# Kernel optimization log

Hardware: AMD Instinct MI355X
Metric: run time of the kernel (lower is better)

The kernel has to match this reference:

```python
import jax, jax.numpy as jnp
import numpy as np

BETA = 0.001  # commitment loss weight from __init__ default


def setup_inputs() -> dict:
    key = jax.random.key(0)
    k1, k2 = jax.random.split(key)
    N, INPUT_DIM = 8192, 1024
    S, K, D = 32, 1024, 32  # nsplits, num_embeddings, embedding_dim
    z = jax.random.normal(k1, (N, INPUT_DIM), dtype=jnp.float32)
    # Stacked codebook weights: one [K, D] embedding table per split.
    W = jax.random.normal(k2, (S, K, D), dtype=jnp.float32)
    return {"z": z, "W": W}


def reference(z, W):
    N, INPUT_DIM = z.shape
    S, K, D = W.shape
    zc = z.reshape(N, S, D)  # per-split chunks, matches torch.chunk(z, S, -1)
    # Squared euclidean distances ||z||^2 + ||w||^2 - 2 z.w  -> [N, S, K]
    d2 = (
        jnp.sum(zc * zc, axis=-1, keepdims=True)
        + jnp.sum(W * W, axis=-1)[None, :, :]
        - 2.0 * jnp.einsum("nsd,skd->nsk", zc, W)
    )
    idx = jnp.argmin(d2, axis=-1)  # [N, S]
    # Gather nearest codes: W[s, idx[n, s]] -> [N, S, D]
    zq = W[jnp.arange(S)[None, :], idx]
    # Sum over splits of per-split mse means; equal split sizes so this is
    # S * mean over the whole tensor.
    sg = jax.lax.stop_gradient
    loss = S * (
        jnp.mean((sg(zq) - zc) ** 2) + BETA * jnp.mean((zq - sg(zc)) ** 2)
    )
    # Straight-through estimator
    zq_st = zc + sg(zq - zc)
    return zq_st.reshape(N, INPUT_DIM), loss
```

## Files before the change

kernel.cpp:

```cpp
#include <hip/hip_runtime.h>
#include <math.h>

#define NN 8192
#define SS 32
#define DD 32
#define KK 1024
#define OUT_ELEMS ((size_t)NN * SS * DD)

#define LOSS_SCALE (32.0f * 1.001f / 8388608.0f)

typedef _Float16 half8 __attribute__((ext_vector_type(8)));
typedef float   floatx4 __attribute__((ext_vector_type(4)));

#define NTILES 64
#define RG 2
#define WAVES 16
#define BLK_ROWS (WAVES * RG * 16)
#define NBLOCKS ((NN / BLK_ROWS) * SS)


#define W2P_OFF  4096
#define WHP_OFF  (W2P_OFF + SS * KK * 4)
#define WLP_OFF  (WHP_OFF + SS * KK * DD * 2)

typedef const __attribute__((address_space(1))) void* gas_p;
typedef __attribute__((address_space(3))) void* las_p;

__device__ __forceinline__ void gll16(const void* g, void* l) {
    __builtin_amdgcn_global_load_lds((gas_p)g, (las_p)l, 16, 0, 0);
}
__device__ __forceinline__ void gll4(const void* g, void* l) {
    __builtin_amdgcn_global_load_lds((gas_p)g, (las_p)l, 4, 0, 0);
}

__global__ __launch_bounds__(256) void w_pre(const float* __restrict__ W,
                                             _Float16* __restrict__ WhP,
                                             _Float16* __restrict__ WlP,
                                             float* __restrict__ w2P) {
    const int u    = blockIdx.x * 256 + threadIdx.x;
    const int s    = u >> 12;
    const int g    = (u >> 6) & 63;
    const int l    = u & 63;
    const int col  = l & 15;
    const int quad = l >> 4;
    const int k    = g * 16 + col;
    const float* src = W + ((size_t)s * KK + k) * DD + quad * 8;
    const float4 va = ((const float4*)src)[0];
    const float4 vb = ((const float4*)src)[1];
    const float v[8] = {va.x, va.y, va.z, va.w, vb.x, vb.y, vb.z, vb.w};
    half8 h8, l8; float ps = 0.0f;
    #pragma unroll
    for (int j = 0; j < 8; ++j) {
        const float x = v[j];
        ps = fmaf(x, x, ps);
        const _Float16 h = (_Float16)x;
        h8[j] = h;
        l8[j] = (_Float16)(x - (float)h);
    }
    ps += __shfl_xor(ps, 16, 64);
    ps += __shfl_xor(ps, 32, 64);
    *(half8*)(WhP + (size_t)u * 8) = h8;
    *(half8*)(WlP + (size_t)u * 8) = l8;
    if (quad == 0) w2P[s * KK + k] = ps;
}

__global__ __launch_bounds__(1024, 4) void vq_fused(const float* __restrict__ z,
                                                    const float* __restrict__ W,
                                                    const _Float16* __restrict__ WhP,
                                                    const _Float16* __restrict__ WlP,
                                                    const float* __restrict__ w2P,
                                                    float* __restrict__ out,
                                                    float* __restrict__ part) {
    __shared__ _Float16 bufH[NTILES][64][8];
    __shared__ _Float16 bufL[NTILES][64][8];
    __shared__ float    w2b[KK];
    __shared__ int      lds_idx[WAVES][32];
    __shared__ float    lds_part[WAVES];

    const int s    = blockIdx.x & (SS - 1);
    const int n0b  = (blockIdx.x >> 5) * BLK_ROWS;
    const int tid  = threadIdx.x;
    const int wv   = tid >> 6;
    const int lane = tid & 63;
    const int col  = lane & 15;
    const int quad = lane >> 4;

    const float* __restrict__ Ws = W + (size_t)s * KK * DD;
    const int n0w = n0b + wv * (RG * 16);

    {
        const char* gH = (const char*)(WhP + (size_t)s * (NTILES * 512));
        const char* gL = (const char*)(WlP + (size_t)s * (NTILES * 512));
        char* lH = (char*)&bufH[0][0][0];
        char* lL = (char*)&bufL[0][0][0];
        const int wvB = wv * 1024;
        #pragma unroll
        for (int i = 0; i < 4; ++i) {
            const int off = i * 16384 + wvB;
            gll16(gH + off + lane * 16, lH + off);
            gll16(gL + off + lane * 16, lL + off);
        }
        const float* g2 = w2P + (size_t)s * KK + wv * 64;
        gll4(g2 + lane, (char*)w2b + wv * 256);
    }

    half8 zh[RG], zl[RG];
    #pragma unroll
    for (int rg = 0; rg < RG; ++rg) {
        const float* zp = z + (size_t)(n0w + rg * 16 + col) * (SS * DD) + s * DD + quad * 8;
        const float4 va = ((const float4*)zp)[0];
        const float4 vb = ((const float4*)zp)[1];
        const float src[8] = {va.x, va.y, va.z, va.w, vb.x, vb.y, vb.z, vb.w};
        #pragma unroll
        for (int j = 0; j < 8; ++j) {
            const float v = -2.0f * src[j];
            const _Float16 h = (_Float16)v;
            zh[rg][j] = h;
            zl[rg][j] = (_Float16)(v - (float)h);
        }
    }

    floatx4 best[RG];
    int bi[RG][4];
    #pragma unroll
    for (int rg = 0; rg < RG; ++rg) {
        best[rg] = (floatx4){INFINITY, INFINITY, INFINITY, INFINITY};
        bi[rg][0] = bi[rg][1] = bi[rg][2] = bi[rg][3] = 0;
    }

    __syncthreads();

    #pragma unroll 8
    for (int tt = 0; tt < NTILES; ++tt) {
        const half8 bh = *(const half8*)&bufH[tt][lane][0];
        const half8 bl = *(const half8*)&bufL[tt][lane][0];
        const float w2v = w2b[tt * 16 + col];
        const floatx4 c0 = {w2v, w2v, w2v, w2v};
        __builtin_amdgcn_s_setprio(1);
        floatx4 a0 = __builtin_amdgcn_mfma_f32_16x16x32_f16(zh[0], bh, c0, 0, 0, 0);
        floatx4 a1 = __builtin_amdgcn_mfma_f32_16x16x32_f16(zh[1], bh, c0, 0, 0, 0);
        a0 = __builtin_amdgcn_mfma_f32_16x16x32_f16(zl[0], bh, a0, 0, 0, 0);
        a1 = __builtin_amdgcn_mfma_f32_16x16x32_f16(zl[1], bh, a1, 0, 0, 0);
        a0 = __builtin_amdgcn_mfma_f32_16x16x32_f16(zh[0], bl, a0, 0, 0, 0);
        a1 = __builtin_amdgcn_mfma_f32_16x16x32_f16(zh[1], bl, a1, 0, 0, 0);
        __builtin_amdgcn_s_setprio(0);
        #pragma unroll
        for (int i = 0; i < 4; ++i) {
            if (a0[i] < best[0][i]) { best[0][i] = a0[i]; bi[0][i] = tt; }
            if (a1[i] < best[1][i]) { best[1][i] = a1[i]; bi[1][i] = tt; }
        }
    }

    #pragma unroll
    for (int rg = 0; rg < RG; ++rg) {
        #pragma unroll
        for (int i = 0; i < 4; ++i) {
            float v = best[rg][i];
            int   k = bi[rg][i] * 16 + col;
            #pragma unroll
            for (int m = 1; m < 16; m <<= 1) {
                const float vo = __shfl_xor(v, m, 64);
                const int   ko = __shfl_xor(k, m, 64);
                if (vo < v || (vo == v && ko < k)) { v = vo; k = ko; }
            }
            if (col == 0) lds_idx[wv][rg * 16 + quad * 4 + i] = k;
        }
    }
    __syncthreads();

    const int r  = lane & 31;
    const int dh = (lane >> 5) * 16;
    const int krow = lds_idx[wv][r];
    const float* wsrc = Ws + (size_t)krow * DD + dh;
    const size_t zoff = (size_t)(n0w + r) * (SS * DD) + s * DD + dh;
    const float* zsrc = z + zoff;
    float* od = out + zoff;
    float sq = 0.0f;
    #pragma unroll
    for (int cc = 0; cc < 4; ++cc) {
        const float4 wq = ((const float4*)wsrc)[cc];
        const float4 zv = ((const float4*)zsrc)[cc];
        const float d0 = wq.x - zv.x, d1 = wq.y - zv.y;
        const float d2 = wq.z - zv.z, d3 = wq.w - zv.w;
        sq = fmaf(d0, d0, sq); sq = fmaf(d1, d1, sq);
        sq = fmaf(d2, d2, sq); sq = fmaf(d3, d3, sq);
        ((float4*)od)[cc] = wq;
    }
    #pragma unroll
    for (int off = 32; off > 0; off >>= 1) sq += __shfl_down(sq, off, 64);

    if (lane == 0) lds_part[wv] = sq;
    __syncthreads();
    if (tid == 0) {
        float t = 0.0f;
        #pragma unroll
        for (int w = 0; w < WAVES; ++w) t += lds_part[w];
        part[blockIdx.x] = t;
    }
}

__global__ __launch_bounds__(256) void vq_loss(const float* __restrict__ part,
                                               float* __restrict__ out) {
    __shared__ float l[4];
    const int tid = threadIdx.x;
    float sum = 0.0f;
    #pragma unroll
    for (int i = 0; i < NBLOCKS / 256; ++i) sum += part[tid + i * 256];
    #pragma unroll
    for (int off = 32; off > 0; off >>= 1) sum += __shfl_down(sum, off, 64);
    if ((tid & 63) == 0) l[tid >> 6] = sum;
    __syncthreads();
    if (tid == 0) out[OUT_ELEMS] = (l[0] + l[1] + l[2] + l[3]) * LOSS_SCALE;
}

extern "C" void kernel_launch(void* const* d_in, const int* in_sizes, int n_in,
                              void* d_out, int out_size, void* d_ws, size_t ws_size,
                              hipStream_t stream) {
    const float* z = (const float*)d_in[0];
    const float* W = (const float*)d_in[1];
    float* out  = (float*)d_out;

    char* ws = (char*)d_ws;
    float*    part = (float*)ws;
    float*    w2P  = (float*)(ws + W2P_OFF);
    _Float16* WhP  = (_Float16*)(ws + WHP_OFF);
    _Float16* WlP  = (_Float16*)(ws + WLP_OFF);

    w_pre<<<dim3(512), dim3(256), 0, stream>>>(W, WhP, WlP, w2P);
    vq_fused<<<dim3(NBLOCKS), dim3(1024), 0, stream>>>(z, W, WhP, WlP, w2P, out, part);
    vq_loss<<<dim3(1), dim3(256), 0, stream>>>(part, out);
}
```

Baseline: 157.3 us.

## Switch distance MFMA from 16x16x32 to 32x32x16 tiles per wave

Replaces the pair of 16x16x32 f16 MFMA row groups with a single 32x32x16 MFMA tile per wave. Each wave covers 32 rows by 32 codes per step over 32 code groups, and the W half/low-part packing is rearranged to the matching layout. The per-tile loop overhead, LDS reads and argmin compare count per code are meant to drop, and the larger MFMA shape may have better throughput. In exchange the 16-element accumulator and the 32-lane cross-lane argmin reduction use more registers and shuffles. The w2 norm is now computed from a separate full-row read in the prep kernel instead of a shuffle reduction.

```diff
diff --git a/kernel.cpp b/kernel.cpp
--- a/kernel.cpp
+++ b/kernel.cpp
@@ -9,13 +9,13 @@
 
 #define LOSS_SCALE (32.0f * 1.001f / 8388608.0f)
 
-typedef _Float16 half8 __attribute__((ext_vector_type(8)));
-typedef float   floatx4 __attribute__((ext_vector_type(4)));
-
-#define NTILES 64
-#define RG 2
+typedef _Float16 half8  __attribute__((ext_vector_type(8)));
+typedef float   floatx4  __attribute__((ext_vector_type(4)));
+typedef float   floatx16 __attribute__((ext_vector_type(16)));
+
+#define NTILES 32
 #define WAVES 16
-#define BLK_ROWS (WAVES * RG * 16)
+#define BLK_ROWS (WAVES * 32)
 #define NBLOCKS ((NN / BLK_ROWS) * SS)
 
 
@@ -32,36 +32,47 @@
 __device__ __forceinline__ void gll4(const void* g, void* l) {
     __builtin_amdgcn_global_load_lds((gas_p)g, (las_p)l, 4, 0, 0);
 }
+
+#define MFMA32(a, b, c) __builtin_amdgcn_mfma_f32_32x32x16_f16((a), (b), (c), 0, 0, 0)
 
 __global__ __launch_bounds__(256) void w_pre(const float* __restrict__ W,
                                              _Float16* __restrict__ WhP,
                                              _Float16* __restrict__ WlP,
                                              float* __restrict__ w2P) {
-    const int u    = blockIdx.x * 256 + threadIdx.x;
-    const int s    = u >> 12;
-    const int g    = (u >> 6) & 63;
-    const int l    = u & 63;
-    const int col  = l & 15;
-    const int quad = l >> 4;
-    const int k    = g * 16 + col;
-    const float* src = W + ((size_t)s * KK + k) * DD + quad * 8;
+    const int u  = blockIdx.x * 256 + threadIdx.x;
+    const int s  = u >> 12;
+    const int r  = u & 4095;
+    const int g  = r >> 7;
+    const int q  = (r >> 6) & 1;
+    const int l  = u & 63;
+    const int k  = g * 32 + (l & 31);
+    const int db = q * 16 + (l >> 5) * 8;
+    const float* src = W + ((size_t)s * KK + k) * DD + db;
     const float4 va = ((const float4*)src)[0];
     const float4 vb = ((const float4*)src)[1];
     const float v[8] = {va.x, va.y, va.z, va.w, vb.x, vb.y, vb.z, vb.w};
-    half8 h8, l8; float ps = 0.0f;
+    half8 h8, l8;
     #pragma unroll
     for (int j = 0; j < 8; ++j) {
         const float x = v[j];
-        ps = fmaf(x, x, ps);
         const _Float16 h = (_Float16)x;
         h8[j] = h;
         l8[j] = (_Float16)(x - (float)h);
     }
-    ps += __shfl_xor(ps, 16, 64);
-    ps += __shfl_xor(ps, 32, 64);
     *(half8*)(WhP + (size_t)u * 8) = h8;
     *(half8*)(WlP + (size_t)u * 8) = l8;
-    if (quad == 0) w2P[s * KK + k] = ps;
+
+    if (u < SS * KK) {
+        const float* row = W + (size_t)u * DD;
+        float ps = 0.0f;
+        #pragma unroll
+        for (int c = 0; c < 8; ++c) {
+            const float4 w4 = ((const float4*)row)[c];
+            ps = fmaf(w4.x, w4.x, ps); ps = fmaf(w4.y, w4.y, ps);
+            ps = fmaf(w4.z, w4.z, ps); ps = fmaf(w4.w, w4.w, ps);
+        }
+        w2P[u] = ps;
+    }
 }
 
 __global__ __launch_bounds__(1024, 4) void vq_fused(const float* __restrict__ z,
@@ -71,8 +82,8 @@
                                                     const float* __restrict__ w2P,
                                                     float* __restrict__ out,
                                                     float* __restrict__ part) {
-    __shared__ _Float16 bufH[NTILES][64][8];
-    __shared__ _Float16 bufL[NTILES][64][8];
+    __shared__ _Float16 bufH[NTILES][2][64][8];
+    __shared__ _Float16 bufL[NTILES][2][64][8];
     __shared__ float    w2b[KK];
     __shared__ int      lds_idx[WAVES][32];
     __shared__ float    lds_part[WAVES];
@@ -82,17 +93,17 @@
     const int tid  = threadIdx.x;
     const int wv   = tid >> 6;
     const int lane = tid & 63;
-    const int col  = lane & 15;
-    const int quad = lane >> 4;
+    const int rowa = lane & 31;
+    const int q5   = lane >> 5;
 
     const float* __restrict__ Ws = W + (size_t)s * KK * DD;
-    const int n0w = n0b + wv * (RG * 16);
+    const int n0w = n0b + wv * 32;
 
     {
-        const char* gH = (const char*)(WhP + (size_t)s * (NTILES * 512));
-        const char* gL = (const char*)(WlP + (size_t)s * (NTILES * 512));
-        char* lH = (char*)&bufH[0][0][0];
-        char* lL = (char*)&bufL[0][0][0];
+        const char* gH = (const char*)(WhP + (size_t)s * (NTILES * 2 * 512));
+        const char* gL = (const char*)(WlP + (size_t)s * (NTILES * 2 * 512));
+        char* lH = (char*)&bufH[0][0][0][0];
+        char* lL = (char*)&bufL[0][0][0][0];
         const int wvB = wv * 1024;
         #pragma unroll
         for (int i = 0; i < 4; ++i) {
@@ -104,72 +115,72 @@
         gll4(g2 + lane, (char*)w2b + wv * 256);
     }
 
-    half8 zh[RG], zl[RG];
-    #pragma unroll
-    for (int rg = 0; rg < RG; ++rg) {
-        const float* zp = z + (size_t)(n0w + rg * 16 + col) * (SS * DD) + s * DD + quad * 8;
+    half8 zh0, zl0, zh1, zl1;
+    {
+        const float* zp = z + (size_t)(n0w + rowa) * (SS * DD) + s * DD + q5 * 8;
         const float4 va = ((const float4*)zp)[0];
         const float4 vb = ((const float4*)zp)[1];
-        const float src[8] = {va.x, va.y, va.z, va.w, vb.x, vb.y, vb.z, vb.w};
+        const float4 vc = ((const float4*)(zp + 16))[0];
+        const float4 vd = ((const float4*)(zp + 16))[1];
+        const float s0[8] = {va.x, va.y, va.z, va.w, vb.x, vb.y, vb.z, vb.w};
+        const float s1[8] = {vc.x, vc.y, vc.z, vc.w, vd.x, vd.y, vd.z, vd.w};
         #pragma unroll
         for (int j = 0; j < 8; ++j) {
-            const float v = -2.0f * src[j];
-            const _Float16 h = (_Float16)v;
-            zh[rg][j] = h;
-            zl[rg][j] = (_Float16)(v - (float)h);
-        }
-    }
-
-    floatx4 best[RG];
-    int bi[RG][4];
-    #pragma unroll
-    for (int rg = 0; rg < RG; ++rg) {
-        best[rg] = (floatx4){INFINITY, INFINITY, INFINITY, INFINITY};
-        bi[rg][0] = bi[rg][1] = bi[rg][2] = bi[rg][3] = 0;
-    }
-
-    __syncthreads();
-
-    #pragma unroll 8
-    for (int tt = 0; tt < NTILES; ++tt) {
-        const half8 bh = *(const half8*)&bufH[tt][lane][0];
-        const half8 bl = *(const half8*)&bufL[tt][lane][0];
-        const float w2v = w2b[tt * 16 + col];
-        const floatx4 c0 = {w2v, w2v, w2v, w2v};
-        __builtin_amdgcn_s_setprio(1);
-        floatx4 a0 = __builtin_amdgcn_mfma_f32_16x16x32_f16(zh[0], bh, c0, 0, 0, 0);
-        floatx4 a1 = __builtin_amdgcn_mfma_f32_16x16x32_f16(zh[1], bh, c0, 0, 0, 0);
-        a0 = __builtin_amdgcn_mfma_f32_16x16x32_f16(zl[0], bh, a0, 0, 0, 0);
-        a1 = __builtin_amdgcn_mfma_f32_16x16x32_f16(zl[1], bh, a1, 0, 0, 0);
-        a0 = __builtin_amdgcn_mfma_f32_16x16x32_f16(zh[0], bl, a0, 0, 0, 0);
-        a1 = __builtin_amdgcn_mfma_f32_16x16x32_f16(zh[1], bl, a1, 0, 0, 0);
-        __builtin_amdgcn_s_setprio(0);
-        #pragma unroll
-        for (int i = 0; i < 4; ++i) {
-            if (a0[i] < best[0][i]) { best[0][i] = a0[i]; bi[0][i] = tt; }
-            if (a1[i] < best[1][i]) { best[1][i] = a1[i]; bi[1][i] = tt; }
-        }
-    }
-
-    #pragma unroll
-    for (int rg = 0; rg < RG; ++rg) {
-        #pragma unroll
-        for (int i = 0; i < 4; ++i) {
-            float v = best[rg][i];
-            int   k = bi[rg][i] * 16 + col;
-            #pragma unroll
-            for (int m = 1; m < 16; m <<= 1) {
-                const float vo = __shfl_xor(v, m, 64);
-                const int   ko = __shfl_xor(k, m, 64);
-                if (vo < v || (vo == v && ko < k)) { v = vo; k = ko; }
-            }
-            if (col == 0) lds_idx[wv][rg * 16 + quad * 4 + i] = k;
-        }
-    }
-    __syncthreads();
-
-    const int r  = lane & 31;
-    const int dh = (lane >> 5) * 16;
+            const float v0 = -2.0f * s0[j];
+            const _Float16 h0 = (_Float16)v0;
+            zh0[j] = h0; zl0[j] = (_Float16)(v0 - (float)h0);
+            const float v1 = -2.0f * s1[j];
+            const _Float16 h1 = (_Float16)v1;
+            zh1[j] = h1; zl1[j] = (_Float16)(v1 - (float)h1);
+        }
+    }
+
+    floatx16 best;
+    int bi[16];
+    #pragma unroll
+    for (int i = 0; i < 16; ++i) { best[i] = INFINITY; bi[i] = 0; }
+
+    __syncthreads();
+
+    #pragma unroll 2
+    for (int g = 0; g < NTILES; ++g) {
+        const half8 bh0 = *(const half8*)&bufH[g][0][lane][0];
+        const half8 bh1 = *(const half8*)&bufH[g][1][lane][0];
+        const half8 bl0 = *(const half8*)&bufL[g][0][lane][0];
+        const half8 bl1 = *(const half8*)&bufL[g][1][lane][0];
+        const float w2v = w2b[g * 32 + rowa];
+        floatx16 c0;
+        #pragma unroll
+        for (int i = 0; i < 16; ++i) c0[i] = w2v;
+        floatx16 acc;
+        acc = MFMA32(zh0, bh0, c0);
+        acc = MFMA32(zh1, bh1, acc);
+        acc = MFMA32(zl0, bh0, acc);
+        acc = MFMA32(zl1, bh1, acc);
+        acc = MFMA32(zh0, bl0, acc);
+        acc = MFMA32(zh1, bl1, acc);
+        #pragma unroll
+        for (int i = 0; i < 16; ++i) {
+            if (acc[i] < best[i]) { best[i] = acc[i]; bi[i] = g; }
+        }
+    }
+
+    #pragma unroll
+    for (int i = 0; i < 16; ++i) {
+        float v = best[i];
+        int   k = bi[i] * 32 + rowa;
+        #pragma unroll
+        for (int m = 1; m < 32; m <<= 1) {
+            const float vo = __shfl_xor(v, m, 64);
+            const int   ko = __shfl_xor(k, m, 64);
+            if (vo < v || (vo == v && ko < k)) { v = vo; k = ko; }
+        }
+        if (rowa == 0) lds_idx[wv][(i & 3) + 8 * (i >> 2) + 4 * q5] = k;
+    }
+    __syncthreads();
+
+    const int r  = rowa;
+    const int dh = q5 * 16;
     const int krow = lds_idx[wv][r];
     const float* wsrc = Ws + (size_t)krow * DD + dh;
     const size_t zoff = (size_t)(n0w + r) * (SS * DD) + s * DD + dh;
```

Measured after the change: 168.9 us. +7.4%, slower.

## Interleave hi/lo codebook tiles and software-pipeline LDS reads with inline asm

Applied to the files above, without the earlier changes.

Codebook hi and lo fp16 halves are now interleaved per tile in one workspace buffer and one LDS array, so a single base address and immediate offsets cover both. The distance loop is hand-pipelined: ds_read_b128/ds_read_b32 are issued via inline asm four tiles ahead with explicit lgkmcnt waits. Each tile's argmin compare is deferred by one tile so it overlaps the next tile's MFMAs. The aim is to hide LDS latency and compare work behind MFMA issue. The cost is fragile inline asm and manual scheduling that may fight the compiler.

```diff
diff --git a/kernel.cpp b/kernel.cpp
--- a/kernel.cpp
+++ b/kernel.cpp
@@ -9,19 +9,17 @@
 
 #define LOSS_SCALE (32.0f * 1.001f / 8388608.0f)
 
-typedef _Float16 half8 __attribute__((ext_vector_type(8)));
+typedef _Float16 half8  __attribute__((ext_vector_type(8)));
 typedef float   floatx4 __attribute__((ext_vector_type(4)));
 
 #define NTILES 64
-#define RG 2
 #define WAVES 16
-#define BLK_ROWS (WAVES * RG * 16)
+#define BLK_ROWS (WAVES * 32)
 #define NBLOCKS ((NN / BLK_ROWS) * SS)
 
 
 #define W2P_OFF  4096
-#define WHP_OFF  (W2P_OFF + SS * KK * 4)
-#define WLP_OFF  (WHP_OFF + SS * KK * DD * 2)
+#define WP_OFF   (W2P_OFF + SS * KK * 4)
 
 typedef const __attribute__((address_space(1))) void* gas_p;
 typedef __attribute__((address_space(3))) void* las_p;
@@ -33,9 +31,10 @@
     __builtin_amdgcn_global_load_lds((gas_p)g, (las_p)l, 4, 0, 0);
 }
 
+#define MFMA16(a, b, c) __builtin_amdgcn_mfma_f32_16x16x32_f16((a), (b), (c), 0, 0, 0)
+
 __global__ __launch_bounds__(256) void w_pre(const float* __restrict__ W,
-                                             _Float16* __restrict__ WhP,
-                                             _Float16* __restrict__ WlP,
+                                             _Float16* __restrict__ WP,
                                              float* __restrict__ w2P) {
     const int u    = blockIdx.x * 256 + threadIdx.x;
     const int s    = u >> 12;
@@ -59,20 +58,19 @@
     }
     ps += __shfl_xor(ps, 16, 64);
     ps += __shfl_xor(ps, 32, 64);
-    *(half8*)(WhP + (size_t)u * 8) = h8;
-    *(half8*)(WlP + (size_t)u * 8) = l8;
+    _Float16* base = WP + ((size_t)(s * 64 + g) * 2) * 512;
+    *(half8*)(base + l * 8) = h8;
+    *(half8*)(base + 512 + l * 8) = l8;
     if (quad == 0) w2P[s * KK + k] = ps;
 }
 
 __global__ __launch_bounds__(1024, 4) void vq_fused(const float* __restrict__ z,
                                                     const float* __restrict__ W,
-                                                    const _Float16* __restrict__ WhP,
-                                                    const _Float16* __restrict__ WlP,
+                                                    const _Float16* __restrict__ WP,
                                                     const float* __restrict__ w2P,
                                                     float* __restrict__ out,
                                                     float* __restrict__ part) {
-    __shared__ _Float16 bufH[NTILES][64][8];
-    __shared__ _Float16 bufL[NTILES][64][8];
+    __shared__ _Float16 bufHL[NTILES][2][64][8];
     __shared__ float    w2b[KK];
     __shared__ int      lds_idx[WAVES][32];
     __shared__ float    lds_part[WAVES];
@@ -86,86 +84,134 @@
     const int quad = lane >> 4;
 
     const float* __restrict__ Ws = W + (size_t)s * KK * DD;
-    const int n0w = n0b + wv * (RG * 16);
+    const int n0w = n0b + wv * 32;
 
     {
-        const char* gH = (const char*)(WhP + (size_t)s * (NTILES * 512));
-        const char* gL = (const char*)(WlP + (size_t)s * (NTILES * 512));
-        char* lH = (char*)&bufH[0][0][0];
-        char* lL = (char*)&bufL[0][0][0];
+        const char* gW = (const char*)(WP + (size_t)s * (NTILES * 2 * 512));
+        char* lW = (char*)&bufHL[0][0][0][0];
         const int wvB = wv * 1024;
         #pragma unroll
-        for (int i = 0; i < 4; ++i) {
+        for (int i = 0; i < 8; ++i) {
             const int off = i * 16384 + wvB;
-            gll16(gH + off + lane * 16, lH + off);
-            gll16(gL + off + lane * 16, lL + off);
+            gll16(gW + off + lane * 16, lW + off);
         }
         const float* g2 = w2P + (size_t)s * KK + wv * 64;
         gll4(g2 + lane, (char*)w2b + wv * 256);
     }
 
-    half8 zh[RG], zl[RG];
-    #pragma unroll
-    for (int rg = 0; rg < RG; ++rg) {
-        const float* zp = z + (size_t)(n0w + rg * 16 + col) * (SS * DD) + s * DD + quad * 8;
-        const float4 va = ((const float4*)zp)[0];
-        const float4 vb = ((const float4*)zp)[1];
-        const float src[8] = {va.x, va.y, va.z, va.w, vb.x, vb.y, vb.z, vb.w};
+    half8 zh0, zl0, zh1, zl1;
+    {
+        const float* zp0 = z + (size_t)(n0w + col) * (SS * DD) + s * DD + quad * 8;
+        const float* zp1 = zp0 + 16 * (SS * DD);
+        const float4 va = ((const float4*)zp0)[0];
+        const float4 vb = ((const float4*)zp0)[1];
+        const float4 vc = ((const float4*)zp1)[0];
+        const float4 vd = ((const float4*)zp1)[1];
+        const float s0[8] = {va.x, va.y, va.z, va.w, vb.x, vb.y, vb.z, vb.w};
+        const float s1[8] = {vc.x, vc.y, vc.z, vc.w, vd.x, vd.y, vd.z, vd.w};
         #pragma unroll
         for (int j = 0; j < 8; ++j) {
-            const float v = -2.0f * src[j];
-            const _Float16 h = (_Float16)v;
-            zh[rg][j] = h;
-            zl[rg][j] = (_Float16)(v - (float)h);
+            const float v0 = -2.0f * s0[j];
+            const _Float16 h0 = (_Float16)v0;
+            zh0[j] = h0; zl0[j] = (_Float16)(v0 - (float)h0);
+            const float v1 = -2.0f * s1[j];
+            const _Float16 h1 = (_Float16)v1;
+            zh1[j] = h1; zl1[j] = (_Float16)(v1 - (float)h1);
         }
     }
 
-    floatx4 best[RG];
-    int bi[RG][4];
-    #pragma unroll
-    for (int rg = 0; rg < RG; ++rg) {
-        best[rg] = (floatx4){INFINITY, INFINITY, INFINITY, INFINITY};
-        bi[rg][0] = bi[rg][1] = bi[rg][2] = bi[rg][3] = 0;
-    }
-
-    __syncthreads();
-
-    #pragma unroll 8
-    for (int tt = 0; tt < NTILES; ++tt) {
-        const half8 bh = *(const half8*)&bufH[tt][lane][0];
-        const half8 bl = *(const half8*)&bufL[tt][lane][0];
-        const float w2v = w2b[tt * 16 + col];
-        const floatx4 c0 = {w2v, w2v, w2v, w2v};
-        __builtin_amdgcn_s_setprio(1);
-        floatx4 a0 = __builtin_amdgcn_mfma_f32_16x16x32_f16(zh[0], bh, c0, 0, 0, 0);
-        floatx4 a1 = __builtin_amdgcn_mfma_f32_16x16x32_f16(zh[1], bh, c0, 0, 0, 0);
-        a0 = __builtin_amdgcn_mfma_f32_16x16x32_f16(zl[0], bh, a0, 0, 0, 0);
-        a1 = __builtin_amdgcn_mfma_f32_16x16x32_f16(zl[1], bh, a1, 0, 0, 0);
-        a0 = __builtin_amdgcn_mfma_f32_16x16x32_f16(zh[0], bl, a0, 0, 0, 0);
-        a1 = __builtin_amdgcn_mfma_f32_16x16x32_f16(zh[1], bl, a1, 0, 0, 0);
-        __builtin_amdgcn_s_setprio(0);
-        #pragma unroll
-        for (int i = 0; i < 4; ++i) {
-            if (a0[i] < best[0][i]) { best[0][i] = a0[i]; bi[0][i] = tt; }
-            if (a1[i] < best[1][i]) { best[1][i] = a1[i]; bi[1][i] = tt; }
-        }
-    }
-
-    #pragma unroll
-    for (int rg = 0; rg < RG; ++rg) {
-        #pragma unroll
-        for (int i = 0; i < 4; ++i) {
-            float v = best[rg][i];
-            int   k = bi[rg][i] * 16 + col;
-            #pragma unroll
-            for (int m = 1; m < 16; m <<= 1) {
-                const float vo = __shfl_xor(v, m, 64);
-                const int   ko = __shfl_xor(k, m, 64);
-                if (vo < v || (vo == v && ko < k)) { v = vo; k = ko; }
-            }
-            if (col == 0) lds_idx[wv][rg * 16 + quad * 4 + i] = k;
-        }
-    }
+    floatx4 best0, best1;
+    int bi0[4], bi1[4];
+    best0 = best1 = (floatx4){INFINITY, INFINITY, INFINITY, INFINITY};
+    bi0[0] = bi0[1] = bi0[2] = bi0[3] = 0;
+    bi1[0] = bi1[1] = bi1[2] = bi1[3] = 0;
+
+    __syncthreads();
+
+    unsigned hladdr = (unsigned)(unsigned long long)(las_p)&bufHL[0][0][0][0]
+                      + (unsigned)(lane * 16);
+    unsigned w2addr = (unsigned)(unsigned long long)(las_p)&w2b[0]
+                      + (unsigned)(col * 4);
+
+#define ISSUE(FH, FL, FW, HO, LO, WO)                                       \
+    asm volatile("ds_read_b128 %0, %3 offset:%c5\n\t"                       \
+                 "ds_read_b128 %1, %3 offset:%c6\n\t"                       \
+                 "ds_read_b32  %2, %4 offset:%c7"                           \
+                 : "=&v"(FH), "=&v"(FL), "=&v"(FW)                          \
+                 : "v"(hladdr), "v"(w2addr), "i"(HO), "i"(LO), "i"(WO))
+
+#define WAITL(N) do {                                                       \
+    asm volatile("s_waitcnt lgkmcnt(%c0)" :: "i"(N) : "memory");            \
+    __builtin_amdgcn_sched_barrier(0);                                      \
+} while (0)
+
+#define MTILE(FH, FL, FW, A0, A1) do {                                      \
+    const floatx4 c0_ = {FW, FW, FW, FW};                                   \
+    A0 = MFMA16(zh0, FH, c0_);                                              \
+    A1 = MFMA16(zh1, FH, c0_);                                              \
+    A0 = MFMA16(zl0, FH, A0);                                               \
+    A1 = MFMA16(zl1, FH, A1);                                               \
+    A0 = MFMA16(zh0, FL, A0);                                               \
+    A1 = MFMA16(zh1, FL, A1);                                               \
+} while (0)
+
+#define CTILE(P0, P1, TK) do {                                              \
+    const int tk_ = (TK);                                                   \
+    _Pragma("unroll")                                                       \
+    for (int i_ = 0; i_ < 4; ++i_) {   \
+        if (P0[i_] < best0[i_]) { best0[i_] = P0[i_]; bi0[i_] = tk_; }      \
+        if (P1[i_] < best1[i_]) { best1[i_] = P1[i_]; bi1[i_] = tk_; }      \
+    }                                                                       \
+} while (0)
+
+    half8 f0h, f0l, f1h, f1l, f2h, f2l, f3h, f3l;
+    float f0w, f1w, f2w, f3w;
+    floatx4 aA0, aA1, aB0, aB1;
+    aB0 = aB1 = (floatx4){INFINITY, INFINITY, INFINITY, INFINITY};
+
+    ISSUE(f0h, f0l, f0w, 0, 1024, 0);
+    ISSUE(f1h, f1l, f1w, 2048, 3072, 64);
+
+    int t4 = 0;
+    #pragma unroll 1
+    for (int g = 0; g < 15; ++g) {
+        WAITL(3); ISSUE(f2h, f2l, f2w, 4096, 5120, 128);
+        MTILE(f0h, f0l, f0w, aA0, aA1); CTILE(aB0, aB1, t4 - 1);
+        WAITL(3); ISSUE(f3h, f3l, f3w, 6144, 7168, 192);
+        MTILE(f1h, f1l, f1w, aB0, aB1); CTILE(aA0, aA1, t4);
+        WAITL(3); ISSUE(f0h, f0l, f0w, 8192, 9216, 256);
+        MTILE(f2h, f2l, f2w, aA0, aA1); CTILE(aB0, aB1, t4 + 1);
+        WAITL(3); ISSUE(f1h, f1l, f1w, 10240, 11264, 320);
+        MTILE(f3h, f3l, f3w, aB0, aB1); CTILE(aA0, aA1, t4 + 2);
+        hladdr += 8192; w2addr += 256; t4 += 4;
+    }
+    WAITL(3); ISSUE(f2h, f2l, f2w, 4096, 5120, 128);
+    MTILE(f0h, f0l, f0w, aA0, aA1); CTILE(aB0, aB1, 59);
+    WAITL(3); ISSUE(f3h, f3l, f3w, 6144, 7168, 192);
+    MTILE(f1h, f1l, f1w, aB0, aB1); CTILE(aA0, aA1, 60);
+    WAITL(3);
+    MTILE(f2h, f2l, f2w, aA0, aA1); CTILE(aB0, aB1, 61);
+    WAITL(0);
+    MTILE(f3h, f3l, f3w, aB0, aB1); CTILE(aA0, aA1, 62);
+    CTILE(aB0, aB1, 63);
+
+#define REDUCE(BEST, BI, RG) do {                                           \
+    _Pragma("unroll")                                                       \
+    for (int i = 0; i < 4; ++i) {                                           \
+        float v = BEST[i];                                                  \
+        int   k = BI[i] * 16 + col;                                         \
+        _Pragma("unroll")                                                   \
+        for (int m = 1; m < 16; m <<= 1) {                                  \
+            const float vo = __shfl_xor(v, m, 64);                          \
+            const int   ko = __shfl_xor(k, m, 64);                          \
+            if (vo < v || (vo == v && ko < k)) { v = vo; k = ko; }          \
+        }                                                                   \
+        if (col == 0) lds_idx[wv][(RG) * 16 + quad * 4 + i] = k;            \
+    }                                                                       \
+} while (0)
+
+    REDUCE(best0, bi0, 0);
+    REDUCE(best1, bi1, 1);
     __syncthreads();
 
     const int r  = lane & 31;
@@ -223,10 +269,9 @@
     char* ws = (char*)d_ws;
     float*    part = (float*)ws;
     float*    w2P  = (float*)(ws + W2P_OFF);
-    _Float16* WhP  = (_Float16*)(ws + WHP_OFF);
-    _Float16* WlP  = (_Float16*)(ws + WLP_OFF);
-
-    w_pre<<<dim3(512), dim3(256), 0, stream>>>(W, WhP, WlP, w2P);
-    vq_fused<<<dim3(NBLOCKS), dim3(1024), 0, stream>>>(z, W, WhP, WlP, w2P, out, part);
+    _Float16* WP   = (_Float16*)(ws + WP_OFF);
+
+    w_pre<<<dim3(512), dim3(256), 0, stream>>>(W, WP, w2P);
+    vq_fused<<<dim3(NBLOCKS), dim3(1024), 0, stream>>>(z, W, WP, w2P, out, part);
     vq_loss<<<dim3(1), dim3(256), 0, stream>>>(part, out);
 }
```

Measured after the change: 154.0 us. 1.02x faster.
